# Performance work log

Hardware: AMD Instinct MI355X
Metric: run time of the kernel (lower is better)

## Reference

```python
import jax, jax.numpy as jnp
import numpy as np
from jax import lax

NX, NY = 6, 6
NB = NX * NY            # 36 blocks
B, S = 64, 256          # batch, sample_count
EPS = 1e-6

def build_edges(nx, ny):
    edges = []
    for i in range(nx):
        for j in range(ny):
            for dx, dy in [(-1, 0), (0, -1), (0, 1), (1, 0)]:
                x, y = i + dx, j + dy
                if 0 <= x < nx and 0 <= y < ny:
                    edges.append((j * nx + i, y * nx + x))
    return np.array(edges, np.int32)   # (120, 2)

EDGES_NP = build_edges(NX, NY)
NE = len(EDGES_NP)  # 120

def setup_inputs() -> dict:
    key = jax.random.key(0)
    ks = jax.random.split(key, 24)
    f32 = jnp.float32
    d = {
        "image":      jax.random.normal(ks[0], (B, 1, 32, 32), f32),
        "edge_noise": jax.random.uniform(ks[1], (B, S, NE), f32),
        "u_s":        jax.random.uniform(ks[2], (B, S, NB), f32),
        "u_d":        jax.random.uniform(ks[3], (B, S, NB), f32),
        # CNN params (OIHW)
        "cw1": jax.random.normal(ks[4], (32, 1, 5, 5), f32) * 0.05,
        "cb1": jnp.zeros((32,), f32),
        "cw2": jax.random.normal(ks[5], (32, 32, 5, 5), f32) * 0.05,
        "cb2": jnp.zeros((32,), f32),
        "cw3": jax.random.normal(ks[6], (64, 32, 5, 5), f32) * 0.05,
        "cb3": jnp.zeros((64,), f32),
        "cw4": jax.random.normal(ks[7], (64, 64, 5, 5), f32) * 0.05,
        "cb4": jnp.zeros((64,), f32),
        # is_connected MLP
        "wc1": jax.random.normal(ks[8], (256, 256), f32) * 0.05,
        "bc1": jnp.zeros((256,), f32),
        "wc2": jax.random.normal(ks[9], (256, NE), f32) * 0.05,
        "bc2": jnp.zeros((NE,), f32),
        # is_endpoint MLP
        "we1": jax.random.normal(ks[10], (256, 256), f32) * 0.05,
        "be1": jnp.zeros((256,), f32),
        "we2": jax.random.normal(ks[11], (256, NB), f32) * 0.05,
        "be2": jnp.zeros((NB,), f32),
        "edges": jnp.asarray(EDGES_NP),  # (NE, 2) int32, constants
    }
    return d

def _conv(x, w, b):
    y = lax.conv_general_dilated(x, w, (1, 1), 'VALID',
                                 dimension_numbers=('NCHW', 'OIHW', 'NCHW'))
    return y + b[None, :, None, None]

def _pool2(x):
    return lax.reduce_window(x, -jnp.inf, lax.max, (1, 1, 2, 2), (1, 1, 2, 2), 'VALID')

def reference(image, edge_noise, u_s, u_d,
              cw1, cb1, cw2, cb2, cw3, cb3, cw4, cb4,
              wc1, bc1, wc2, bc2, we1, be1, we2, be2, edges):
    # ---- CNN feature extractor ----
    h = _conv(image, cw1, cb1)
    h = _conv(h, cw2, cb2)
    h = _pool2(h)
    h = _conv(h, cw3, cb3)
    h = _conv(h, cw4, cb4)
    h = _pool2(h)
    emb = h.reshape(h.shape[0], -1)              # (B, 256)

    # ---- heads ----
    p_conn = jax.nn.sigmoid(jax.nn.relu(emb @ wc1 + bc1) @ wc2 + bc2)   # (B, NE)
    p_ep   = jax.nn.sigmoid(jax.nn.relu(emb @ we1 + be1) @ we2 + be2)   # (B, NB)

    pc = jnp.clip(p_conn, EPS, 1.0 - EPS)
    pe = jnp.clip(p_ep, EPS, 1.0 - EPS)
    cat = pe / pe.sum(-1, keepdims=True)
    logcat = jnp.log(cat)                        # (B, NB)

    # ---- Monte-Carlo sampling (ISED blackbox) ----
    conn = (edge_noise < pc[:, None, :]).astype(pc.dtype)               # (B,S,NE) Bernoulli
    g_s = -jnp.log(-jnp.log(jnp.clip(u_s, EPS, 1.0 - EPS)))
    g_d = -jnp.log(-jnp.log(jnp.clip(u_d, EPS, 1.0 - EPS)))
    s_idx = jnp.argmax(logcat[:, None, :] + g_s, axis=-1)               # (B,S) categorical
    d_idx = jnp.argmax(logcat[:, None, :] + g_d, axis=-1)               # (B,S)

    # ---- batched BFS reachability via boolean matrix squaring ----
    oh_u = jax.nn.one_hot(edges[:, 0], NB, dtype=pc.dtype)              # (NE, NB)
    oh_v = jax.nn.one_hot(edges[:, 1], NB, dtype=pc.dtype)
    e_sym = jnp.einsum('eu,ev->euv', oh_u, oh_v) + jnp.einsum('eu,ev->evu', oh_u, oh_v)
    A = jnp.minimum(jnp.einsum('bse,euv->bsuv', conn, e_sym), 1.0)      # (B,S,36,36)

    R = jnp.minimum(A + jnp.eye(NB, dtype=A.dtype), 1.0)
    for _ in range(6):                           # (I+A)^(2^6), covers path len<=36
        R = jnp.minimum(R @ R, 1.0)
    P = jnp.minimum(A @ R, 1.0)                  # paths of length >= 1 (BFS semantics)

    Pv = jnp.take_along_axis(P, s_idx[:, :, None, None], axis=2)[:, :, 0, :]  # (B,S,36)
    exists = (jnp.take_along_axis(Pv, d_idx[:, :, None], axis=2)[:, :, 0] > 0.5).astype(pc.dtype)  # (B,S)

    # ---- sample-probability weighting (differentiable ISED estimator) ----
    logw = (conn * jnp.log(pc)[:, None, :] + (1.0 - conn) * jnp.log1p(-pc)[:, None, :]).sum(-1)
    logw = logw + jnp.take_along_axis(logcat, s_idx, axis=1) \
                + jnp.take_along_axis(logcat, d_idx, axis=1)            # (B,S)
    w = jax.nn.softmax(logw, axis=1)
    p1 = (w * exists).sum(axis=1)                # P(path exists)
    return jnp.stack([1.0 - p1, p1], axis=-1)    # (B, 2)
```

## Files before the change

### kernel.cpp

```cpp
#include <hip/hip_runtime.h>

typedef unsigned long long u64;
#define EPSF 1e-6f

__global__ __launch_bounds__(512) void k_conv1(const float* __restrict__ img,
                                               const float* __restrict__ cw1,
                                               const float* __restrict__ cb1,
                                               float* __restrict__ c1) {
  int slab = blockIdx.x, b = blockIdx.y;
  __shared__ float simg[32 * 33];
  for (int k = threadIdx.x; k < 1024; k += 512) {
    int y = k >> 5, x = k & 31;
    simg[y * 33 + x] = img[b * 1024 + k];
  }
  int half = threadIdx.x >> 8;
  int u = threadIdx.x & 255;
  int ocl = u >> 5;
  int x = u & 31;
  int oc = slab * 8 + ocl;
  int y0 = half * 14;
  float w[25];
#pragma unroll
  for (int k = 0; k < 25; ++k) w[k] = cw1[oc * 25 + k];
  float bias = cb1[oc];
  __syncthreads();
  if (x < 28) {
    float acc[5];
#pragma unroll
    for (int k = 0; k < 5; ++k) acc[k] = bias;
    float* outp = c1 + (b * 32 + oc) * 784 + x;
#pragma unroll
    for (int rr = 0; rr < 18; ++rr) {
      int r = y0 + rr;
      float in[5];
#pragma unroll
      for (int c = 0; c < 5; ++c) in[c] = simg[r * 33 + x + c];
#pragma unroll
      for (int ky = 0; ky < 5; ++ky) {
        if (rr < ky || rr - ky > 13) continue;
        int slot = (rr - ky) % 5;
#pragma unroll
        for (int kx = 0; kx < 5; ++kx)
          acc[slot] = fmaf(w[ky * 5 + kx], in[kx], acc[slot]);
      }
      if (rr >= 4) {
        int slot = (rr - 4) % 5;
        outp[(y0 + rr - 4) * 28] = acc[slot];
        acc[slot] = bias;
      }
    }
  }
}

__global__ __launch_bounds__(1024) void k_conv2(const float* __restrict__ c1,
                                                const float* __restrict__ cw2,
                                                const float* __restrict__ cb2,
                                                float* __restrict__ p1w) {
  int ocq = blockIdx.x, b = blockIdx.y;
  __shared__ float smem[25984];
  int t = threadIdx.x;
  if (t < 784) {
    int row = t / 28, col = t % 28;
    int lofs = row * 29 + col;
    const float* src = c1 + (size_t)b * 25088 + t;
#pragma unroll
    for (int ic = 0; ic < 32; ++ic) smem[ic * 812 + lofs] = src[ic * 784];
  }
  int w = __builtin_amdgcn_readfirstlane(t >> 6);
  int opair = w & 3;
  int icq = w >> 2;
  int l = t & 63;
  int py = l >> 3, px = l & 7;
  int oc0 = ocq * 8 + opair * 2;
  const float* wApt = cw2 + (size_t)oc0 * 800 + icq * 200;
  const float* wBpt = wApt + 800;
  float acc[2][9];
#pragma unroll
  for (int j = 0; j < 2; ++j)
#pragma unroll
    for (int e = 0; e < 9; ++e) acc[j][e] = 0.f;
  __syncthreads();

  const float* base0 = smem + icq * 8 * 812 + (3 * py) * 29 + 3 * px;
#pragma unroll
  for (int ic = 0; ic < 8; ++ic) {
    float wa[25], wb[25];
#pragma unroll
    for (int k = 0; k < 25; ++k) { wa[k] = wApt[ic * 25 + k]; wb[k] = wBpt[ic * 25 + k]; }
    const float* base = base0 + ic * 812;
#pragma unroll
    for (int rr = 0; rr < 7; ++rr) {
      float win[7];
#pragma unroll
      for (int m = 0; m < 7; ++m) win[m] = base[rr * 29 + m];
#pragma unroll
      for (int i = 0; i < 3; ++i) {
        if (i > rr || rr - i > 4) continue;
        int ky = rr - i;
#pragma unroll
        for (int kx = 0; kx < 5; ++kx) {
#pragma unroll
          for (int jj = 0; jj < 3; ++jj) {
            acc[0][i * 3 + jj] = fmaf(wa[ky * 5 + kx], win[jj + kx], acc[0][i * 3 + jj]);
            acc[1][i * 3 + jj] = fmaf(wb[ky * 5 + kx], win[jj + kx], acc[1][i * 3 + jj]);
          }
        }
      }
    }
  }

  __syncthreads();
  float* slots = smem;
  float* cbuf = smem + 9216;
  int chunk = opair * 2 * 576 + l * 9;
  if (icq >= 2) {
    float* d = slots + (icq - 2) * 4608 + chunk;
#pragma unroll
    for (int j = 0; j < 2; ++j)
#pragma unroll
      for (int e = 0; e < 9; ++e) d[j * 576 + e] = acc[j][e];
  }
  __syncthreads();
  if (icq < 2) {
    const float* s = slots + icq * 4608 + chunk;
#pragma unroll
    for (int j = 0; j < 2; ++j)
#pragma unroll
      for (int e = 0; e < 9; ++e) acc[j][e] += s[j * 576 + e];
  }
  __syncthreads();
  if (icq == 1) {
    float* d = slots + chunk;
#pragma unroll
    for (int j = 0; j < 2; ++j)
#pragma unroll
      for (int e = 0; e < 9; ++e) d[j * 576 + e] = acc[j][e];
  }
  __syncthreads();
  if (icq == 0) {
    const float* s = slots + chunk;
#pragma unroll
    for (int j = 0; j < 2; ++j) {
      float bias = cb2[oc0 + j];
#pragma unroll
      for (int i = 0; i < 3; ++i)
#pragma unroll
        for (int jj = 0; jj < 3; ++jj)
          cbuf[(opair * 2 + j) * 576 + (3 * py + i) * 24 + 3 * px + jj] =
              acc[j][i * 3 + jj] + s[j * 576 + i * 3 + jj] + bias;
    }
  }
  __syncthreads();
  for (int k = t; k < 1152; k += 1024) {
    int o = k / 144, rem = k % 144;
    int PY = rem / 12, PX = rem % 12;
    const float* b0 = cbuf + o * 576 + (2 * PY) * 24 + 2 * PX;
    float m = fmaxf(fmaxf(b0[0], b0[1]), fmaxf(b0[24], b0[25]));
    p1w[((size_t)b * 32 + ocq * 8 + o) * 144 + PY * 12 + PX] = m;
  }
}

__global__ __launch_bounds__(256) void k_conv3(const float* __restrict__ p1w,
                                               const float* __restrict__ cw3,
                                               const float* __restrict__ cb3,
                                               float* __restrict__ c3) {
  int oc8 = blockIdx.x, b = blockIdx.y;
  __shared__ float smem[11008];
  float* w3s = smem;
  float* ins = smem + 6400;
  int t = threadIdx.x;
  {
    const float4* src = (const float4*)(p1w + b * 32 * 144);
    float4* dst = (float4*)ins;
    for (int k = t; k < 1152; k += 256) dst[k] = src[k];
  }
  {
    const float4* src = (const float4*)(cw3 + oc8 * 8 * 800);
    for (int k4 = t; k4 < 1600; k4 += 256) {
      float4 v = src[k4];
      float vv[4] = {v.x, v.y, v.z, v.w};
      int k = k4 * 4;
#pragma unroll
      for (int r = 0; r < 4; ++r) {
        int kk = k + r;
        int o = kk / 800, rest = kk % 800;
        w3s[rest * 8 + o] = vv[r];
      }
    }
  }
  int g = t >> 4, p = t & 15;
  int ocg = p >> 3, row = p & 7;
  float acc[4][8];
#pragma unroll
  for (int j = 0; j < 4; ++j)
#pragma unroll
    for (int c = 0; c < 8; ++c) acc[j][c] = 0.f;
  __syncthreads();
#pragma unroll
  for (int icl = 0; icl < 2; ++icl) {
    int ic = g + icl * 16;
#pragma unroll
    for (int ky = 0; ky < 5; ++ky) {
      const float4* rp = (const float4*)(ins + ic * 144 + (row + ky) * 12);
      float win[12];
#pragma unroll
      for (int q = 0; q < 3; ++q) {
        float4 v = rp[q];
        win[4 * q] = v.x; win[4 * q + 1] = v.y; win[4 * q + 2] = v.z; win[4 * q + 3] = v.w;
      }
      const float* wb = w3s + (ic * 25 + ky * 5) * 8 + ocg * 4;
#pragma unroll
      for (int kx = 0; kx < 5; ++kx) {
        float wq[4];
        *(float4*)wq = *(const float4*)(wb + kx * 8);
#pragma unroll
        for (int c = 0; c < 8; ++c) {
#pragma unroll
          for (int j = 0; j < 4; ++j) acc[j][c] = fmaf(wq[j], win[c + kx], acc[j][c]);
        }
      }
    }
  }
  float* buf = smem;
  __syncthreads();
  if (g >= 8) {
    float* d = buf + (g - 8) * 512 + p * 32;
#pragma unroll
    for (int j = 0; j < 4; ++j)
#pragma unroll
      for (int c = 0; c < 8; ++c) d[j * 8 + c] = acc[j][c];
  }
  __syncthreads();
  if (g < 8) {
    const float* s = buf + g * 512 + p * 32;
#pragma unroll
    for (int j = 0; j < 4; ++j)
#pragma unroll
      for (int c = 0; c < 8; ++c) acc[j][c] += s[j * 8 + c];
  }
  __syncthreads();
  if (g >= 4 && g < 8) {
    float* d = buf + (g - 4) * 512 + p * 32;
#pragma unroll
    for (int j = 0; j < 4; ++j)
#pragma unroll
      for (int c = 0; c < 8; ++c) d[j * 8 + c] = acc[j][c];
  }
  __syncthreads();
  if (g < 4) {
    const float* s = buf + g * 512 + p * 32;
#pragma unroll
    for (int j = 0; j < 4; ++j)
#pragma unroll
      for (int c = 0; c < 8; ++c) acc[j][c] += s[j * 8 + c];
  }
  __syncthreads();
  if (g == 2 || g == 3) {
    float* d = buf + (g - 2) * 512 + p * 32;
#pragma unroll
    for (int j = 0; j < 4; ++j)
#pragma unroll
      for (int c = 0; c < 8; ++c) d[j * 8 + c] = acc[j][c];
  }
  __syncthreads();
  if (g < 2) {
    const float* s = buf + g * 512 + p * 32;
#pragma unroll
    for (int j = 0; j < 4; ++j)
#pragma unroll
      for (int c = 0; c < 8; ++c) acc[j][c] += s[j * 8 + c];
  }
  __syncthreads();
  if (g == 1) {
    float* d = buf + p * 32;
#pragma unroll
    for (int j = 0; j < 4; ++j)
#pragma unroll
      for (int c = 0; c < 8; ++c) d[j * 8 + c] = acc[j][c];
  }
  __syncthreads();
  if (g == 0) {
    const float* s = buf + p * 32;
#pragma unroll
    for (int j = 0; j < 4; ++j) {
      float bias = cb3[oc8 * 8 + ocg * 4 + j];
      float4 v0, v1;
      v0.x = acc[j][0] + s[j * 8 + 0] + bias; v0.y = acc[j][1] + s[j * 8 + 1] + bias;
      v0.z = acc[j][2] + s[j * 8 + 2] + bias; v0.w = acc[j][3] + s[j * 8 + 3] + bias;
      v1.x = acc[j][4] + s[j * 8 + 4] + bias; v1.y = acc[j][5] + s[j * 8 + 5] + bias;
      v1.z = acc[j][6] + s[j * 8 + 6] + bias; v1.w = acc[j][7] + s[j * 8 + 7] + bias;
      float* op = c3 + (b * 64 + oc8 * 8 + ocg * 4 + j) * 64 + row * 8;
      *(float4*)op = v0; *(float4*)(op + 4) = v1;
    }
  }
}

__global__ __launch_bounds__(256) void k_conv4(const float* __restrict__ c3,
                                               const float* __restrict__ cw4,
                                               const float* __restrict__ cb4,
                                               float* __restrict__ emb) {
  int oc8 = blockIdx.x, b = blockIdx.y;
  __shared__ float smem[17152];
  float* w4s = smem;
  float* ins = smem + 12800;
  int t = threadIdx.x;
  {
    const float4* src = (const float4*)(c3 + b * 4096);
    for (int k = t; k < 1024; k += 256) {
      int ic = k >> 4, q = k & 15;
      *(float4*)(ins + ic * 68 + q * 4) = src[k];
    }
  }
  {
    const float4* src = (const float4*)(cw4 + oc8 * 8 * 1600);
    for (int k4 = t; k4 < 3200; k4 += 256) {
      float4 v = src[k4];
      float vv[4] = {v.x, v.y, v.z, v.w};
      int k = k4 * 4;
#pragma unroll
      for (int r = 0; r < 4; ++r) {
        int kk = k + r;
        int o = kk / 1600, rest = kk % 1600;
        w4s[rest * 8 + o] = vv[r];
      }
    }
  }
  int g = t >> 3, p = t & 7;
  int ocg = p >> 2, row = p & 3;
  float acc[4][4];
#pragma unroll
  for (int j = 0; j < 4; ++j)
#pragma unroll
    for (int c = 0; c < 4; ++c) acc[j][c] = 0.f;
  __syncthreads();
#pragma unroll
  for (int icl = 0; icl < 2; ++icl) {
    int ic = g + icl * 32;
#pragma unroll
    for (int ky = 0; ky < 5; ++ky) {
      const float4* rp = (const float4*)(ins + ic * 68 + (row + ky) * 8);
      float win[8];
#pragma unroll
      for (int q = 0; q < 2; ++q) {
        float4 v = rp[q];
        win[4 * q] = v.x; win[4 * q + 1] = v.y; win[4 * q + 2] = v.z; win[4 * q + 3] = v.w;
      }
      const float* wb = w4s + (ic * 25 + ky * 5) * 8 + ocg * 4;
#pragma unroll
      for (int kx = 0; kx < 5; ++kx) {
        float wq[4];
        *(float4*)wq = *(const float4*)(wb + kx * 8);
#pragma unroll
        for (int c = 0; c < 4; ++c) {
#pragma unroll
          for (int j = 0; j < 4; ++j) acc[j][c] = fmaf(wq[j], win[c + kx], acc[j][c]);
        }
      }
    }
  }
  float* buf = smem;
#pragma unroll
  for (int half = 16; half >= 1; half >>= 1) {
    __syncthreads();
    if (g >= half && g < 2 * half) {
      float* d = buf + (g - half) * 128 + p * 16;
#pragma unroll
      for (int j = 0; j < 4; ++j)
#pragma unroll
        for (int c = 0; c < 4; ++c) d[j * 4 + c] = acc[j][c];
    }
    __syncthreads();
    if (g < half) {
      const float* s = buf + g * 128 + p * 16;
#pragma unroll
      for (int j = 0; j < 4; ++j)
#pragma unroll
        for (int c = 0; c < 4; ++c) acc[j][c] += s[j * 4 + c];
    }
  }
  float* pb = buf + 2048;
  if (g == 0) {
#pragma unroll
    for (int j = 0; j < 4; ++j) {
      float bias = cb4[oc8 * 8 + ocg * 4 + j];
#pragma unroll
      for (int c = 0; c < 4; ++c) pb[(ocg * 4 + j) * 16 + row * 4 + c] = acc[j][c] + bias;
    }
  }
  __syncthreads();
  if (t < 32) {
    int o = t >> 2, q = t & 3, py = q >> 1, px = q & 1;
    const float* b0 = pb + o * 16 + (2 * py) * 4 + 2 * px;
    float m = fmaxf(fmaxf(b0[0], b0[1]), fmaxf(b0[4], b0[5]));
    emb[b * 256 + (oc8 * 8 + o) * 4 + py * 2 + px] = m;
  }
}

__global__ __launch_bounds__(256) void k_heads(const float* __restrict__ emb,
    const float* __restrict__ wc1, const float* __restrict__ bc1,
    const float* __restrict__ wc2, const float* __restrict__ bc2,
    const float* __restrict__ we1, const float* __restrict__ be1,
    const float* __restrict__ we2, const float* __restrict__ be2,
    float* __restrict__ pcw, float* __restrict__ lpcw,
    float* __restrict__ l1mw, float* __restrict__ lcatw) {
  int head = blockIdx.x, b = blockIdx.y;
  int t = threadIdx.x;
  __shared__ float e_s[256], h_s[256];
  __shared__ float aux;
  e_s[t] = emb[b * 256 + t];
  __syncthreads();
  const float* W1 = head ? we1 : wc1;
  const float* B1 = head ? be1 : bc1;
  float s = B1[t];
  for (int i = 0; i < 256; i += 4) {
    s = fmaf(e_s[i], W1[i * 256 + t], s);
    s = fmaf(e_s[i + 1], W1[(i + 1) * 256 + t], s);
    s = fmaf(e_s[i + 2], W1[(i + 2) * 256 + t], s);
    s = fmaf(e_s[i + 3], W1[(i + 3) * 256 + t], s);
  }
  h_s[t] = fmaxf(s, 0.f);
  __syncthreads();
  int NO = head ? 36 : 120;
  const float* W2 = head ? we2 : wc2;
  const float* B2 = head ? be2 : bc2;
  if (t < NO) {
    float s2 = B2[t];
    for (int i = 0; i < 256; ++i) s2 = fmaf(h_s[i], W2[i * NO + t], s2);
    float p = 1.f / (1.f + expf(-s2));
    p = fminf(fmaxf(p, EPSF), 1.f - EPSF);
    if (head == 0) {
      pcw[b * 120 + t] = p;
      lpcw[b * 120 + t] = logf(p);
      l1mw[b * 120 + t] = log1pf(-p);
    } else {
      e_s[t] = p;
    }
  }
  if (head == 1) {
    __syncthreads();
    if (t == 0) {
      float sm = 0.f;
      for (int j2 = 0; j2 < 36; ++j2) sm += e_s[j2];
      aux = sm;
    }
    __syncthreads();
    if (t < 36) lcatw[b * 36 + t] = logf(e_s[t] / aux);
  }
}

__global__ __launch_bounds__(64) void k_mc1(const float* __restrict__ enoise,
    const float* __restrict__ us, const float* __restrict__ ud,
    const int* __restrict__ edges,
    const float* __restrict__ pcw, const float* __restrict__ lpcw,
    const float* __restrict__ l1mw, const float* __restrict__ lcatw,
    float* __restrict__ lw, float* __restrict__ exx) {
  int chunk = blockIdx.x, b = blockIdx.y, t = threadIdx.x;
  int s = chunk * 64 + t;
  __shared__ __align__(16) float pc_s[120];
  __shared__ __align__(16) float lpc_s[120];
  __shared__ __align__(16) float l1m_s[120];
  __shared__ __align__(16) float lcat_s[36];
  __shared__ __align__(16) int einfo[120];
  for (int k = t; k < 120; k += 64) {
    pc_s[k] = pcw[b * 120 + k];
    lpc_s[k] = lpcw[b * 120 + k];
    l1m_s[k] = l1mw[b * 120 + k];
    int u = edges[2 * k], v = edges[2 * k + 1];
    int d = v - u;
    int isV = (d == 6 || d == -6) ? 1 : 0;
    int pos = d > 0 ? u : v;
    einfo[k] = pos | (isV << 6);
  }
  if (t < 36) lcat_s[t] = lcatw[b * 36 + t];
  __syncthreads();

  float logw = 0.f;
  u64 H = 0, V = 0;
  {
    const float4* np = (const float4*)(enoise + ((size_t)(b * 256 + s)) * 120);
#pragma unroll
    for (int q = 0; q < 30; ++q) {
      float4 nz = np[q];
      float4 p4 = ((const float4*)pc_s)[q];
      float4 lp4 = ((const float4*)lpc_s)[q];
      float4 lm4 = ((const float4*)l1m_s)[q];
      int4 e4 = ((const int4*)einfo)[q];
      float nv[4] = {nz.x, nz.y, nz.z, nz.w};
      float pv[4] = {p4.x, p4.y, p4.z, p4.w};
      float lv[4] = {lp4.x, lp4.y, lp4.z, lp4.w};
      float mv[4] = {lm4.x, lm4.y, lm4.z, lm4.w};
      int ev[4] = {e4.x, e4.y, e4.z, e4.w};
#pragma unroll
      for (int r = 0; r < 4; ++r) {
        bool conn = nv[r] < pv[r];
        logw += conn ? lv[r] : mv[r];
        if (conn) {
          u64 bit = 1ull << (ev[r] & 63);
          if (ev[r] & 64) V |= bit; else H |= bit;
        }
      }
    }
  }
  int si = 0, di = 0;
  {
    const float4* up = (const float4*)(us + ((size_t)(b * 256 + s)) * 36);
    float best = -1e30f;
#pragma unroll
    for (int q = 0; q < 9; ++q) {
      float4 uv = up[q];
      float4 lc4 = ((const float4*)lcat_s)[q];
      float vv[4] = {uv.x, uv.y, uv.z, uv.w};
      float lc[4] = {lc4.x, lc4.y, lc4.z, lc4.w};
#pragma unroll
      for (int r = 0; r < 4; ++r) {
        float u = fminf(fmaxf(vv[r], EPSF), 1.f - EPSF);
        float gq = -logf(-logf(u));
        float val = lc[r] + gq;
        if (val > best) { best = val; si = q * 4 + r; }
      }
    }
  }
  {
    const float4* up = (const float4*)(ud + ((size_t)(b * 256 + s)) * 36);
    float best = -1e30f;
#pragma unroll
    for (int q = 0; q < 9; ++q) {
      float4 uv = up[q];
      float4 lc4 = ((const float4*)lcat_s)[q];
      float vv[4] = {uv.x, uv.y, uv.z, uv.w};
      float lc[4] = {lc4.x, lc4.y, lc4.z, lc4.w};
#pragma unroll
      for (int r = 0; r < 4; ++r) {
        float u = fminf(fmaxf(vv[r], EPSF), 1.f - EPSF);
        float gq = -logf(-logf(u));
        float val = lc[r] + gq;
        if (val > best) { best = val; di = q * 4 + r; }
      }
    }
  }
  logw += lcat_s[si] + lcat_s[di];

  u64 comp = 1ull << si;
  while (true) {
    u64 prev = comp;
    comp |= ((comp & H) << 1) | ((comp >> 1) & H);
    comp |= ((comp & V) << 6) | ((comp >> 6) & V);
    if (comp == prev) break;
  }
  float ex;
  if (si == di) ex = (comp != (1ull << si)) ? 1.f : 0.f;
  else ex = ((comp >> di) & 1ull) ? 1.f : 0.f;

  lw[b * 256 + s] = logw;
  exx[b * 256 + s] = ex;
}

__global__ __launch_bounds__(256) void k_mc2(const float* __restrict__ lw,
                                             const float* __restrict__ exx,
                                             float* __restrict__ out) {
  int b = blockIdx.x, t = threadIdx.x;
  __shared__ float red_s[256];
  float logw = lw[b * 256 + t];
  float ex = exx[b * 256 + t];
  red_s[t] = logw; __syncthreads();
  for (int off = 128; off > 0; off >>= 1) {
    if (t < off) red_s[t] = fmaxf(red_s[t], red_s[t + off]);
    __syncthreads();
  }
  float m = red_s[0]; __syncthreads();
  float evx = expf(logw - m);
  red_s[t] = evx; __syncthreads();
  for (int off = 128; off > 0; off >>= 1) {
    if (t < off) red_s[t] += red_s[t + off];
    __syncthreads();
  }
  float den = red_s[0]; __syncthreads();
  red_s[t] = evx * ex; __syncthreads();
  for (int off = 128; off > 0; off >>= 1) {
    if (t < off) red_s[t] += red_s[t + off];
    __syncthreads();
  }
  if (t == 0) {
    float p1v = red_s[0] / den;
    out[b * 2] = 1.f - p1v;
    out[b * 2 + 1] = p1v;
  }
}

extern "C" void kernel_launch(void* const* d_in, const int* in_sizes, int n_in,
                              void* d_out, int out_size, void* d_ws, size_t ws_size,
                              hipStream_t stream) {
  const float* image = (const float*)d_in[0];
  const float* enoise = (const float*)d_in[1];
  const float* us = (const float*)d_in[2];
  const float* udn = (const float*)d_in[3];
  const float* cw1 = (const float*)d_in[4];
  const float* cb1 = (const float*)d_in[5];
  const float* cw2 = (const float*)d_in[6];
  const float* cb2 = (const float*)d_in[7];
  const float* cw3 = (const float*)d_in[8];
  const float* cb3 = (const float*)d_in[9];
  const float* cw4 = (const float*)d_in[10];
  const float* cb4 = (const float*)d_in[11];
  const float* wc1 = (const float*)d_in[12];
  const float* bc1 = (const float*)d_in[13];
  const float* wc2 = (const float*)d_in[14];
  const float* bc2 = (const float*)d_in[15];
  const float* we1 = (const float*)d_in[16];
  const float* be1 = (const float*)d_in[17];
  const float* we2 = (const float*)d_in[18];
  const float* be2 = (const float*)d_in[19];
  const int* edges = (const int*)d_in[20];

  float* ws = (float*)d_ws;
  float* c1 = ws;
  float* p1w = ws + 1605632;
  float* c3 = ws + 1900544;
  float* emb = ws + 2162688;
  float* pcw = ws + 2179072;
  float* lpcw = ws + 2186752;
  float* l1mw = ws + 2194432;
  float* lcatw = ws + 2202112;
  float* lw = ws + 2204416;
  float* exx = ws + 2220800;
  float* outp = (float*)d_out;

  k_conv1<<<dim3(4, 64), dim3(512), 0, stream>>>(image, cw1, cb1, c1);
  k_conv2<<<dim3(4, 64), dim3(1024), 0, stream>>>(c1, cw2, cb2, p1w);
  k_conv3<<<dim3(8, 64), dim3(256), 0, stream>>>(p1w, cw3, cb3, c3);
  k_conv4<<<dim3(8, 64), dim3(256), 0, stream>>>(c3, cw4, cb4, emb);
  k_heads<<<dim3(2, 64), dim3(256), 0, stream>>>(emb, wc1, bc1, wc2, bc2,
                                                 we1, be1, we2, be2,
                                                 pcw, lpcw, l1mw, lcatw);
  k_mc1<<<dim3(4, 64), dim3(64), 0, stream>>>(enoise, us, udn, edges,
                                              pcw, lpcw, l1mw, lcatw, lw, exx);
  k_mc2<<<dim3(64), dim3(256), 0, stream>>>(lw, exx, outp);
}
```

Baseline: 120.5 us.

## Split conv2 input channels across blocks and reduce partials in a separate pool kernel

The conv2 kernel is split along input channels into two halves. Each block now handles 16 input channels and writes partial sums to a workspace buffer. A new small kernel adds the two partials and the bias, then applies 2x2 max pooling. This doubles the grid from 256 to 512 blocks and halves shared memory per block, which should improve occupancy and CU utilisation on the GPU. The cost is one extra kernel launch plus a global-memory round trip for the partial buffers.

```diff
diff --git a/kernel.cpp b/kernel.cpp
--- a/kernel.cpp
+++ b/kernel.cpp
@@ -52,19 +52,18 @@
   }
 }
 
-__global__ __launch_bounds__(1024) void k_conv2(const float* __restrict__ c1,
-                                                const float* __restrict__ cw2,
-                                                const float* __restrict__ cb2,
-                                                float* __restrict__ p1w) {
-  int ocq = blockIdx.x, b = blockIdx.y;
-  __shared__ float smem[25984];
+__global__ __launch_bounds__(1024) void k_conv2a(const float* __restrict__ c1,
+                                                 const float* __restrict__ cw2,
+                                                 float* __restrict__ part) {
+  int ocq = blockIdx.x, ich = blockIdx.y, b = blockIdx.z;
+  __shared__ float smem[12992];
   int t = threadIdx.x;
   if (t < 784) {
     int row = t / 28, col = t % 28;
     int lofs = row * 29 + col;
-    const float* src = c1 + (size_t)b * 25088 + t;
-#pragma unroll
-    for (int ic = 0; ic < 32; ++ic) smem[ic * 812 + lofs] = src[ic * 784];
+    const float* src = c1 + (size_t)b * 25088 + ich * 16 * 784 + t;
+#pragma unroll
+    for (int ic = 0; ic < 16; ++ic) smem[ic * 812 + lofs] = src[ic * 784];
   }
   int w = __builtin_amdgcn_readfirstlane(t >> 6);
   int opair = w & 3;
@@ -72,7 +71,7 @@
   int l = t & 63;
   int py = l >> 3, px = l & 7;
   int oc0 = ocq * 8 + opair * 2;
-  const float* wApt = cw2 + (size_t)oc0 * 800 + icq * 200;
+  const float* wApt = cw2 + (size_t)oc0 * 800 + (ich * 16 + icq * 4) * 25;
   const float* wBpt = wApt + 800;
   float acc[2][9];
 #pragma unroll
@@ -81,9 +80,9 @@
     for (int e = 0; e < 9; ++e) acc[j][e] = 0.f;
   __syncthreads();
 
-  const float* base0 = smem + icq * 8 * 812 + (3 * py) * 29 + 3 * px;
-#pragma unroll
-  for (int ic = 0; ic < 8; ++ic) {
+  const float* base0 = smem + icq * 4 * 812 + (3 * py) * 29 + 3 * px;
+#pragma unroll
+  for (int ic = 0; ic < 4; ++ic) {
     float wa[25], wb[25];
 #pragma unroll
     for (int k = 0; k < 25; ++k) { wa[k] = wApt[ic * 25 + k]; wb[k] = wBpt[ic * 25 + k]; }
@@ -111,7 +110,6 @@
 
   __syncthreads();
   float* slots = smem;
-  float* cbuf = smem + 9216;
   int chunk = opair * 2 * 576 + l * 9;
   if (icq >= 2) {
     float* d = slots + (icq - 2) * 4608 + chunk;
@@ -139,25 +137,36 @@
   __syncthreads();
   if (icq == 0) {
     const float* s = slots + chunk;
-#pragma unroll
-    for (int j = 0; j < 2; ++j) {
-      float bias = cb2[oc0 + j];
+    float* dst = part + ((size_t)(b * 2 + ich) * 32 + oc0) * 576;
+#pragma unroll
+    for (int j = 0; j < 2; ++j)
 #pragma unroll
       for (int i = 0; i < 3; ++i)
 #pragma unroll
         for (int jj = 0; jj < 3; ++jj)
-          cbuf[(opair * 2 + j) * 576 + (3 * py + i) * 24 + 3 * px + jj] =
-              acc[j][i * 3 + jj] + s[j * 576 + i * 3 + jj] + bias;
-    }
-  }
-  __syncthreads();
-  for (int k = t; k < 1152; k += 1024) {
-    int o = k / 144, rem = k % 144;
-    int PY = rem / 12, PX = rem % 12;
-    const float* b0 = cbuf + o * 576 + (2 * PY) * 24 + 2 * PX;
-    float m = fmaxf(fmaxf(b0[0], b0[1]), fmaxf(b0[24], b0[25]));
-    p1w[((size_t)b * 32 + ocq * 8 + o) * 144 + PY * 12 + PX] = m;
-  }
+          dst[j * 576 + (3 * py + i) * 24 + 3 * px + jj] =
+              acc[j][i * 3 + jj] + s[j * 576 + i * 3 + jj];
+  }
+}
+
+__global__ __launch_bounds__(256) void k_conv2b(const float* __restrict__ part,
+                                                const float* __restrict__ cb2,
+                                                float* __restrict__ p1w) {
+  int idx = blockIdx.x * 256 + threadIdx.x;
+  int img = idx / 4608;
+  int rem = idx % 4608;
+  int oc = rem / 144;
+  int pq = rem % 144;
+  int PY = pq / 12, PX = pq % 12;
+  const float* h0 = part + ((size_t)(img * 2 + 0) * 32 + oc) * 576 + (2 * PY) * 24 + 2 * PX;
+  const float* h1 = h0 + 32 * 576;
+  float bias = cb2[oc];
+  float a = h0[0] + h1[0] + bias;
+  float b2 = h0[1] + h1[1] + bias;
+  float c = h0[24] + h1[24] + bias;
+  float d = h0[25] + h1[25] + bias;
+  float m = fmaxf(fmaxf(a, b2), fmaxf(c, d));
+  p1w[((size_t)img * 32 + oc) * 144 + pq] = m;
 }
 
 __global__ __launch_bounds__(256) void k_conv3(const float* __restrict__ p1w,
@@ -623,10 +632,12 @@
   float* lcatw = ws + 2202112;
   float* lw = ws + 2204416;
   float* exx = ws + 2220800;
+  float* part = ws + 2237184;
   float* outp = (float*)d_out;
 
   k_conv1<<<dim3(4, 64), dim3(512), 0, stream>>>(image, cw1, cb1, c1);
-  k_conv2<<<dim3(4, 64), dim3(1024), 0, stream>>>(c1, cw2, cb2, p1w);
+  k_conv2a<<<dim3(4, 2, 64), dim3(1024), 0, stream>>>(c1, cw2, part);
+  k_conv2b<<<dim3(1152), dim3(256), 0, stream>>>(part, cb2, p1w);
   k_conv3<<<dim3(8, 64), dim3(256), 0, stream>>>(p1w, cw3, cb3, c3);
   k_conv4<<<dim3(8, 64), dim3(256), 0, stream>>>(c3, cw4, cb4, emb);
   k_heads<<<dim3(2, 64), dim3(256), 0, stream>>>(emb, wc1, bc1, wc2, bc2,
```

Result: slower. 125.5 us (+4.2%).
